# Optimization experiments

Hardware: AMD Instinct MI355X
Metric: run time of the kernel (lower is better)

Reference implementation:

```python
import jax, jax.numpy as jnp
import numpy as np

DEPTH = 6
EC_CE_WEIGHT = 1.0
EMB_DIM = 300
NUM_MODALITIES = 6
BATCH = 8192


def setup_inputs() -> dict:
    key = jax.random.key(0)
    ks = jax.random.split(key, DEPTH + 1)
    inp = {"latents": jax.random.normal(ks[0], (NUM_MODALITIES, BATCH, EMB_DIM), dtype=jnp.float32)}
    for i in range(DEPTH):
        inp[f"emb{i}"] = jax.random.normal(ks[i + 1], (2 ** (i + 1), EMB_DIM), dtype=jnp.float32)
    return inp


def _l2norm(x, eps=1e-12):
    # F.normalize(p=2): x / clamp(||x||, min=eps)
    return x / jnp.maximum(jnp.linalg.norm(x, axis=-1, keepdims=True), eps)


def _cos_rows(a, b, eps=1e-8):
    # F.cosine_similarity(dim=1) with eps-clamped norms
    na = jnp.maximum(jnp.linalg.norm(a, axis=1), eps)
    nb = jnp.maximum(jnp.linalg.norm(b, axis=1), eps)
    return jnp.sum(a * b, axis=1) / (na * nb)


def _align(r_in, emb, d):
    # argmin quantization + bidirectional cosine losses + straight-through estimator
    idx = jnp.argmin(d, axis=1)
    q = emb[idx]  # one-hot(encodings) @ emb == gather
    e_loss = 1.0 - jnp.mean(_cos_rows(jax.lax.stop_gradient(q), r_in))
    q_loss = 1.0 - jnp.mean(_cos_rows(q, jax.lax.stop_gradient(r_in)))
    q_st = r_in + jax.lax.stop_gradient(q - r_in)
    return idx, q_st, q_loss + e_loss


def _single_tree(x, embs):
    # x: (B, 300). Sequential over depth levels (routing dependency).
    r = _l2norm(x)
    last_idx = None
    idxs, vecs, losses = [], [], []
    for emb_w in embs:
        emb = _l2norm(emb_w)  # get_tree_node_embedding normalization
        e = _l2norm(emb)      # second normalize inside cal_distance (idempotent)
        d = 1.0 - r @ e.T     # (B, K) cosine distances
        if last_idx is None:
            d_tree = d
        else:
            # only the two children of last level's node are reachable
            cols = jnp.arange(emb.shape[0])[None, :]
            child = (cols == 2 * last_idx[:, None]) | (cols == 2 * last_idx[:, None] + 1)
            d_tree = jnp.where(child, d, jnp.inf)
        idx, q, loss_ec = _align(x, emb, d_tree)
        _, _, loss_ce = _align(emb, x, d_tree.T)
        idxs.append(idx)
        vecs.append(q)
        losses.append(loss_ec + loss_ce * EC_CE_WEIGHT)
        last_idx = idx
    tree_rout = jnp.stack(idxs, axis=1)    # (B, depth)
    vector_rout = jnp.stack(vecs, axis=1)  # (B, depth, 300)
    return tree_rout, vector_rout, jnp.mean(jnp.stack(losses))


def reference(latents, emb0, emb1, emb2, emb3, emb4, emb5):
    embs = (emb0, emb1, emb2, emb3, emb4, emb5)
    tree, vec, loss = jax.vmap(lambda x: _single_tree(x, embs))(latents)
    total_loss = jnp.mean(loss)  # mean over modalities (weight=1.0)
    return tree, vec, total_loss
```

## Files before the change

kernel.cpp:

```cpp
#include <hip/hip_runtime.h>

#define NMOD 6
#define BATCH 8192
#define EMB 300
#define DEPTH 6
#define NROWS 126
#define NPART 32

typedef __attribute__((ext_vector_type(4))) float f32x4;

__device__ __forceinline__ unsigned long long pack_key(double d, int b) {
    unsigned u = __float_as_uint((float)d);
    u = (u & 0x80000000u) ? ~u : (u | 0x80000000u);
    return ((unsigned long long)u << 32) | (unsigned)b;
}

__global__ void prep_kernel(const float* __restrict__ e0, const float* __restrict__ e1,
                            const float* __restrict__ e2, const float* __restrict__ e3,
                            const float* __restrict__ e4, const float* __restrict__ e5,
                            double* __restrict__ e_d, float* __restrict__ e_f,
                            unsigned long long* __restrict__ kpart) {
    const int bid = blockIdx.x;
    const int lane = threadIdx.x;
    if (bid >= NROWS) {
        for (int i = lane; i < NPART * NMOD * NROWS; i += 64) kpart[i] = ~0ull;
        return;
    }
    const float* src;
    if (bid < 2)       src = e0 + (size_t)bid * EMB;
    else if (bid < 6)  src = e1 + (size_t)(bid - 2) * EMB;
    else if (bid < 14) src = e2 + (size_t)(bid - 6) * EMB;
    else if (bid < 30) src = e3 + (size_t)(bid - 14) * EMB;
    else if (bid < 62) src = e4 + (size_t)(bid - 30) * EMB;
    else               src = e5 + (size_t)(bid - 62) * EMB;

    double w[5];
    double ss = 0.0;
    #pragma unroll
    for (int it = 0; it < 5; ++it) {
        int j = lane + it * 64;
        double v = (j < EMB) ? (double)src[j] : 0.0;
        w[it] = v;
        ss += v * v;
    }
    #pragma unroll
    for (int o = 32; o > 0; o >>= 1) ss += __shfl_xor(ss, o);
    double nrm = sqrt(ss);
    if (nrm < 1e-12) nrm = 1e-12;
    #pragma unroll
    for (int it = 0; it < 5; ++it) {
        int j = lane + it * 64;
        if (j < EMB) {
            double v = w[it] / nrm;
            e_d[(size_t)bid * EMB + j] = v;
            e_f[(size_t)bid * EMB + j] = (float)v;
        }
    }
}

__global__ __launch_bounds__(256) void route_kernel(
    const float* __restrict__ latents,
    const double* __restrict__ e_d, const float* __restrict__ e_f,
    float* __restrict__ tree_out, float* __restrict__ vec_out,
    unsigned long long* __restrict__ kpart, double* __restrict__ ecp) {

    __shared__ unsigned long long tbl[NROWS];
    __shared__ double s_ec[4][DEPTH];

    const int tid = threadIdx.x;
    for (int i = tid; i < NROWS; i += 256) tbl[i] = ~0ull;
    __syncthreads();

    const int w = tid >> 6;
    const int lane = tid & 63;
    const int row = blockIdx.x * 4 + w;
    const int m = row >> 13;
    const int b = row & (BATCH - 1);

    const float* x = latents + (size_t)row * EMB;
    double r[5];
    double ss = 0.0;
    #pragma unroll
    for (int it = 0; it < 5; ++it) {
        int j = lane + it * 64;
        double v = (j < EMB) ? (double)x[j] : 0.0;
        r[it] = v;
        ss += v * v;
    }
    #pragma unroll
    for (int o = 32; o > 0; o >>= 1) ss += __shfl_xor(ss, o);
    double nrm = sqrt(ss);
    if (nrm < 1e-12) nrm = 1e-12;
    #pragma unroll
    for (int it = 0; it < 5; ++it) r[it] /= nrm;

    int cur = 0;
    int idxs[DEPTH];
    #pragma unroll
    for (int l = 0; l < DEPTH; ++l) {
        const int base = (2 << l) - 2;
        const int c0 = 2 * cur;
        const size_t g0 = (size_t)(base + c0) * EMB;

        const float* p0 = e_f + g0;
        const float* p1 = p0 + EMB;
        double s0 = 0.0, s1 = 0.0;
        #pragma unroll
        for (int it = 0; it < 5; ++it) {
            int j = lane + it * 64;
            if (j < EMB) {
                double rv = r[it];
                s0 += rv * (double)p0[j];
                s1 += rv * (double)p1[j];
            }
        }
        #pragma unroll
        for (int o = 32; o > 0; o >>= 1) { s0 += __shfl_xor(s0, o); s1 += __shfl_xor(s1, o); }

        if (fabs(s0 - s1) < 1e-3) {
            const double* q0 = e_d + g0;
            const double* q1 = q0 + EMB;
            s0 = 0.0; s1 = 0.0;
            #pragma unroll
            for (int it = 0; it < 5; ++it) {
                int j = lane + it * 64;
                if (j < EMB) {
                    double rv = r[it];
                    s0 += rv * q0[j];
                    s1 += rv * q1[j];
                }
            }
            #pragma unroll
            for (int o = 32; o > 0; o >>= 1) { s0 += __shfl_xor(s0, o); s1 += __shfl_xor(s1, o); }
        }

        double d0 = 1.0 - s0, d1 = 1.0 - s1;
        int sel = (d1 < d0) ? 1 : 0;
        int idx = c0 + sel;
        idxs[l] = idx;
        if (lane == 0) {
            s_ec[w][l] = sel ? d1 : d0;
            atomicMin(&tbl[base + c0],     pack_key(d0, b));
            atomicMin(&tbl[base + c0 + 1], pack_key(d1, b));
        }
        cur = idx;
    }

    #pragma unroll
    for (int l = 0; l < DEPTH; ++l) {
        if (lane == l) {
            __builtin_nontemporal_store((float)idxs[l], &tree_out[(size_t)row * DEPTH + l]);
        }
    }

    #pragma unroll
    for (int l = 0; l < DEPTH; ++l) {
        const int base = (2 << l) - 2;
        const f32x4* src = (const f32x4*)(e_f + (size_t)(base + idxs[l]) * EMB);
        f32x4* dst = (f32x4*)(vec_out + ((size_t)row * DEPTH + l) * EMB);
        for (int i = lane; i < EMB / 4; i += 64) {
            __builtin_nontemporal_store(src[i], &dst[i]);
        }
    }

    __syncthreads();

    const int bm = blockIdx.x & 2047;
    if (tid < DEPTH) {
        double s = s_ec[0][tid] + s_ec[1][tid] + s_ec[2][tid] + s_ec[3][tid];
        ecp[((size_t)m * DEPTH + tid) * 2048 + bm] = s;
    }

    const int part = blockIdx.x & (NPART - 1);
    for (int i = tid; i < NROWS; i += 256) {
        unsigned long long v = tbl[i];
        if (v != ~0ull) atomicMin(&kpart[(size_t)part * (NMOD * NROWS) + m * NROWS + i], v);
    }
}

__global__ void kreduce_kernel(const unsigned long long* __restrict__ kpart,
                               unsigned long long* __restrict__ keys) {
    const int c = blockIdx.x * 256 + threadIdx.x;
    if (c >= NMOD * NROWS) return;
    unsigned long long v = ~0ull;
    #pragma unroll 4
    for (int p = 0; p < NPART; ++p) {
        unsigned long long u = kpart[(size_t)p * (NMOD * NROWS) + c];
        if (u < v) v = u;
    }
    keys[c] = v;
}

__global__ __launch_bounds__(256) void ec_reduce_kernel(const double* __restrict__ ecp,
                                                        double* __restrict__ ec_sum) {
    const int tid = threadIdx.x;
    double s = 0.0;
    for (int i = tid; i < 2048; i += 256) s += ecp[(size_t)blockIdx.x * 2048 + i];
    #pragma unroll
    for (int o = 32; o > 0; o >>= 1) s += __shfl_xor(s, o);
    __shared__ double sw[4];
    if ((tid & 63) == 0) sw[tid >> 6] = s;
    __syncthreads();
    if (tid == 0) ec_sum[blockIdx.x] = sw[0] + sw[1] + sw[2] + sw[3];
}

__global__ void ce_kernel(const float* __restrict__ latents,
                          const double* __restrict__ e_d,
                          const unsigned long long* __restrict__ keys,
                          double* __restrict__ cev) {
    const int tid = threadIdx.x;
    const int w = tid >> 6;
    const int lane = tid & 63;
    const int c = blockIdx.x * 4 + w;
    if (c >= NMOD * NROWS) return;
    const int m = c / NROWS;
    const int g = c % NROWS;
    int K;
    if (g < 2) K = 2;
    else if (g < 6) K = 4;
    else if (g < 14) K = 8;
    else if (g < 30) K = 16;
    else if (g < 62) K = 32;
    else K = 64;

    unsigned long long key = keys[c];
    int b2 = (key == ~0ull) ? 0 : (int)(key & 0xFFFFFFFFull);

    const float* x = latents + ((size_t)m * BATCH + b2) * EMB;
    const double* e = e_d + (size_t)g * EMB;
    double ss = 0.0, dot = 0.0;
    #pragma unroll
    for (int it = 0; it < 5; ++it) {
        int j = lane + it * 64;
        if (j < EMB) {
            double v = (double)x[j];
            ss += v * v;
            dot += v * e[j];
        }
    }
    #pragma unroll
    for (int o = 32; o > 0; o >>= 1) { ss += __shfl_xor(ss, o); dot += __shfl_xor(dot, o); }
    double nx = sqrt(ss);
    if (nx < 1e-8) nx = 1e-8;
    double dd = 1.0 - dot / nx;
    if (lane == 0) cev[c] = 2.0 * dd / (36.0 * (double)K);
}

__global__ __launch_bounds__(256) void final_kernel(const double* __restrict__ ec_sum,
                                                    const double* __restrict__ cev,
                                                    float* __restrict__ loss_out) {
    const int tid = threadIdx.x;
    double s = 0.0;
    for (int i = tid; i < NMOD * NROWS; i += 256) s += cev[i];
    for (int i = tid; i < NMOD * DEPTH; i += 256) s += ec_sum[i] * (2.0 / (36.0 * (double)BATCH));
    #pragma unroll
    for (int o = 32; o > 0; o >>= 1) s += __shfl_xor(s, o);
    __shared__ double sw[4];
    if ((tid & 63) == 0) sw[tid >> 6] = s;
    __syncthreads();
    if (tid == 0) loss_out[0] = (float)(sw[0] + sw[1] + sw[2] + sw[3]);
}

extern "C" void kernel_launch(void* const* d_in, const int* in_sizes, int n_in,
                              void* d_out, int out_size, void* d_ws, size_t ws_size,
                              hipStream_t stream) {
    const float* latents = (const float*)d_in[0];
    const float* e0 = (const float*)d_in[1];
    const float* e1 = (const float*)d_in[2];
    const float* e2 = (const float*)d_in[3];
    const float* e3 = (const float*)d_in[4];
    const float* e4 = (const float*)d_in[5];
    const float* e5 = (const float*)d_in[6];

    float* out = (float*)d_out;
    float* tree_out = out;
    float* vec_out = out + (size_t)NMOD * BATCH * DEPTH;
    float* loss_out = vec_out + (size_t)NMOD * BATCH * DEPTH * EMB;

    char* ws = (char*)d_ws;
    double* e_d = (double*)ws;
    float* e_f = (float*)(ws + 302400);
    unsigned long long* keys = (unsigned long long*)(ws + 453600);
    unsigned long long* kpart = (unsigned long long*)(ws + 459648);
    double* ecp = (double*)(ws + 653184);
    double* cev = (double*)(ws + 1243008);
    double* ec_sum = (double*)(ws + 1249056);

    prep_kernel<<<dim3(NROWS + 1), dim3(64), 0, stream>>>(
        e0, e1, e2, e3, e4, e5, e_d, e_f, kpart);
    route_kernel<<<dim3(NMOD * BATCH / 4), dim3(256), 0, stream>>>(
        latents, e_d, e_f, tree_out, vec_out, kpart, ecp);
    kreduce_kernel<<<dim3((NMOD * NROWS + 255) / 256), dim3(256), 0, stream>>>(kpart, keys);
    ec_reduce_kernel<<<dim3(NMOD * DEPTH), dim3(256), 0, stream>>>(ecp, ec_sum);
    ce_kernel<<<dim3((NMOD * NROWS + 3) / 4), dim3(256), 0, stream>>>(
        latents, e_d, keys, cev);
    final_kernel<<<dim3(1), dim3(256), 0, stream>>>(ec_sum, cev, loss_out);
}
```

Before: 463.7 us.

## Use fp32 vectorized dot products in routing with fp64 fallback; merge reduce kernels

```diff
diff --git a/kernel.cpp b/kernel.cpp
--- a/kernel.cpp
+++ b/kernel.cpp
@@ -9,8 +9,8 @@
 
 typedef __attribute__((ext_vector_type(4))) float f32x4;
 
-__device__ __forceinline__ unsigned long long pack_key(double d, int b) {
-    unsigned u = __float_as_uint((float)d);
+__device__ __forceinline__ unsigned long long pack_key(float d, int b) {
+    unsigned u = __float_as_uint(d);
     u = (u & 0x80000000u) ? ~u : (u | 0x80000000u);
     return ((unsigned long long)u << 32) | (unsigned)b;
 }
@@ -77,22 +77,16 @@
     const int m = row >> 13;
     const int b = row & (BATCH - 1);
 
-    const float* x = latents + (size_t)row * EMB;
-    double r[5];
-    double ss = 0.0;
-    #pragma unroll
-    for (int it = 0; it < 5; ++it) {
-        int j = lane + it * 64;
-        double v = (j < EMB) ? (double)x[j] : 0.0;
-        r[it] = v;
-        ss += v * v;
-    }
-    #pragma unroll
-    for (int o = 32; o > 0; o >>= 1) ss += __shfl_xor(ss, o);
-    double nrm = sqrt(ss);
-    if (nrm < 1e-12) nrm = 1e-12;
-    #pragma unroll
-    for (int it = 0; it < 5; ++it) r[it] /= nrm;
+    const f32x4* x4 = (const f32x4*)(latents + (size_t)row * EMB);
+    const f32x4 zero4 = {0.f, 0.f, 0.f, 0.f};
+    f32x4 xu0 = x4[lane];
+    f32x4 xu1 = (lane < 11) ? x4[64 + lane] : zero4;
+
+    float ssf = xu0[0]*xu0[0] + xu0[1]*xu0[1] + xu0[2]*xu0[2] + xu0[3]*xu0[3]
+              + xu1[0]*xu1[0] + xu1[1]*xu1[1] + xu1[2]*xu1[2] + xu1[3]*xu1[3];
+    #pragma unroll
+    for (int o = 32; o > 0; o >>= 1) ssf += __shfl_xor(ssf, o);
+    const float rinv = 1.0f / fmaxf(sqrtf(ssf), 1e-12f);
 
     int cur = 0;
     int idxs[DEPTH];
@@ -102,46 +96,65 @@
         const int c0 = 2 * cur;
         const size_t g0 = (size_t)(base + c0) * EMB;
 
-        const float* p0 = e_f + g0;
-        const float* p1 = p0 + EMB;
-        double s0 = 0.0, s1 = 0.0;
+        const f32x4* p04 = (const f32x4*)(e_f + g0);
+        const f32x4* p14 = (const f32x4*)(e_f + g0 + EMB);
+        f32x4 a0 = p04[lane];
+        f32x4 b0 = p14[lane];
+        f32x4 a1 = zero4, b1 = zero4;
+        if (lane < 11) { a1 = p04[64 + lane]; b1 = p14[64 + lane]; }
+
+        float t0 = xu0[0]*a0[0] + xu0[1]*a0[1] + xu0[2]*a0[2] + xu0[3]*a0[3]
+                 + xu1[0]*a1[0] + xu1[1]*a1[1] + xu1[2]*a1[2] + xu1[3]*a1[3];
+        float t1 = xu0[0]*b0[0] + xu0[1]*b0[1] + xu0[2]*b0[2] + xu0[3]*b0[3]
+                 + xu1[0]*b1[0] + xu1[1]*b1[1] + xu1[2]*b1[2] + xu1[3]*b1[3];
         #pragma unroll
-        for (int it = 0; it < 5; ++it) {
-            int j = lane + it * 64;
-            if (j < EMB) {
-                double rv = r[it];
-                s0 += rv * (double)p0[j];
-                s1 += rv * (double)p1[j];
-            }
-        }
-        #pragma unroll
-        for (int o = 32; o > 0; o >>= 1) { s0 += __shfl_xor(s0, o); s1 += __shfl_xor(s1, o); }
-
-        if (fabs(s0 - s1) < 1e-3) {
+        for (int o = 32; o > 0; o >>= 1) { t0 += __shfl_xor(t0, o); t1 += __shfl_xor(t1, o); }
+        float s0 = t0 * rinv, s1 = t1 * rinv;
+
+        double d0x, d1x;
+        bool esc = fabsf(s0 - s1) < 1e-3f;
+        if (esc) {
             const double* q0 = e_d + g0;
             const double* q1 = q0 + EMB;
-            s0 = 0.0; s1 = 0.0;
+            double ssd = 0.0, u0 = 0.0, u1 = 0.0;
             #pragma unroll
-            for (int it = 0; it < 5; ++it) {
-                int j = lane + it * 64;
-                if (j < EMB) {
-                    double rv = r[it];
-                    s0 += rv * q0[j];
-                    s1 += rv * q1[j];
+            for (int q = 0; q < 4; ++q) {
+                double xv = (double)xu0[q];
+                ssd += xv * xv;
+                u0 += xv * q0[4 * lane + q];
+                u1 += xv * q1[4 * lane + q];
+            }
+            if (lane < 11) {
+                #pragma unroll
+                for (int q = 0; q < 4; ++q) {
+                    double xv = (double)xu1[q];
+                    ssd += xv * xv;
+                    u0 += xv * q0[256 + 4 * lane + q];
+                    u1 += xv * q1[256 + 4 * lane + q];
                 }
             }
             #pragma unroll
-            for (int o = 32; o > 0; o >>= 1) { s0 += __shfl_xor(s0, o); s1 += __shfl_xor(s1, o); }
-        }
-
-        double d0 = 1.0 - s0, d1 = 1.0 - s1;
-        int sel = (d1 < d0) ? 1 : 0;
+            for (int o = 32; o > 0; o >>= 1) {
+                ssd += __shfl_xor(ssd, o);
+                u0 += __shfl_xor(u0, o);
+                u1 += __shfl_xor(u1, o);
+            }
+            double nd = sqrt(ssd);
+            if (nd < 1e-12) nd = 1e-12;
+            d0x = 1.0 - u0 / nd;
+            d1x = 1.0 - u1 / nd;
+        } else {
+            d0x = (double)(1.0f - s0);
+            d1x = (double)(1.0f - s1);
+        }
+
+        int sel = (d1x < d0x) ? 1 : 0;
         int idx = c0 + sel;
         idxs[l] = idx;
         if (lane == 0) {
-            s_ec[w][l] = sel ? d1 : d0;
-            atomicMin(&tbl[base + c0],     pack_key(d0, b));
-            atomicMin(&tbl[base + c0 + 1], pack_key(d1, b));
+            s_ec[w][l] = sel ? d1x : d0x;
+            atomicMin(&tbl[base + c0],     pack_key((float)d0x, b));
+            atomicMin(&tbl[base + c0 + 1], pack_key((float)d1x, b));
         }
         cur = idx;
     }
@@ -178,30 +191,32 @@
     }
 }
 
-__global__ void kreduce_kernel(const unsigned long long* __restrict__ kpart,
-                               unsigned long long* __restrict__ keys) {
-    const int c = blockIdx.x * 256 + threadIdx.x;
-    if (c >= NMOD * NROWS) return;
-    unsigned long long v = ~0ull;
-    #pragma unroll 4
-    for (int p = 0; p < NPART; ++p) {
-        unsigned long long u = kpart[(size_t)p * (NMOD * NROWS) + c];
-        if (u < v) v = u;
-    }
-    keys[c] = v;
-}
-
-__global__ __launch_bounds__(256) void ec_reduce_kernel(const double* __restrict__ ecp,
-                                                        double* __restrict__ ec_sum) {
+__global__ __launch_bounds__(256) void reduce_kernel(
+    const unsigned long long* __restrict__ kpart, unsigned long long* __restrict__ keys,
+    const double* __restrict__ ecp, double* __restrict__ ec_sum) {
+    const int bid = blockIdx.x;
     const int tid = threadIdx.x;
-    double s = 0.0;
-    for (int i = tid; i < 2048; i += 256) s += ecp[(size_t)blockIdx.x * 2048 + i];
-    #pragma unroll
-    for (int o = 32; o > 0; o >>= 1) s += __shfl_xor(s, o);
-    __shared__ double sw[4];
-    if ((tid & 63) == 0) sw[tid >> 6] = s;
-    __syncthreads();
-    if (tid == 0) ec_sum[blockIdx.x] = sw[0] + sw[1] + sw[2] + sw[3];
+    if (bid < NMOD * DEPTH) {
+        double s = 0.0;
+        for (int i = tid; i < 2048; i += 256) s += ecp[(size_t)bid * 2048 + i];
+        #pragma unroll
+        for (int o = 32; o > 0; o >>= 1) s += __shfl_xor(s, o);
+        __shared__ double sw[4];
+        if ((tid & 63) == 0) sw[tid >> 6] = s;
+        __syncthreads();
+        if (tid == 0) ec_sum[bid] = sw[0] + sw[1] + sw[2] + sw[3];
+    } else {
+        const int c = (bid - NMOD * DEPTH) * 256 + tid;
+        if (c < NMOD * NROWS) {
+            unsigned long long v = ~0ull;
+            #pragma unroll 4
+            for (int p = 0; p < NPART; ++p) {
+                unsigned long long u = kpart[(size_t)p * (NMOD * NROWS) + c];
+                if (u < v) v = u;
+            }
+            keys[c] = v;
+        }
+    }
 }
 
 __global__ void ce_kernel(const float* __restrict__ latents,
@@ -290,8 +305,7 @@
         e0, e1, e2, e3, e4, e5, e_d, e_f, kpart);
     route_kernel<<<dim3(NMOD * BATCH / 4), dim3(256), 0, stream>>>(
         latents, e_d, e_f, tree_out, vec_out, kpart, ecp);
-    kreduce_kernel<<<dim3((NMOD * NROWS + 255) / 256), dim3(256), 0, stream>>>(kpart, keys);
-    ec_reduce_kernel<<<dim3(NMOD * DEPTH), dim3(256), 0, stream>>>(ecp, ec_sum);
+    reduce_kernel<<<dim3(NMOD * DEPTH + 3), dim3(256), 0, stream>>>(kpart, keys, ecp, ec_sum);
     ce_kernel<<<dim3((NMOD * NROWS + 3) / 4), dim3(256), 0, stream>>>(
         latents, e_d, keys, cev);
     final_kernel<<<dim3(1), dim3(256), 0, stream>>>(ec_sum, cev, loss_out);
```

Result: no change. 462.1 us (-0.4%).
